# Kernel optimization log

Measured on AMD Instinct MI355X. Metric: run time of the kernel, lower is better.

Reference implementation:

```python
import jax, jax.numpy as jnp
import numpy as np

BS, C, H, W = 256, 512, 9, 9
D = 9           # spe_kerner (spectral attention kernel size)
SPA_HEAD = 64
HW = H * W      # 81; with spe_head=1, padsize=9 => share_head = 81 = HW
EPS = 1e-5


def _bn(x, p, axis=1):
    # inference-mode BatchNorm; p is (4, C) = [gamma, beta, running_mean, running_var]
    g, b, m, v = p
    sh = [1] * x.ndim; sh[axis] = -1
    return (x - m.reshape(sh)) * (g.reshape(sh) * jax.lax.rsqrt(v.reshape(sh) + EPS)) + b.reshape(sh)


def _conv2d(x, w, groups=1):
    return jax.lax.conv_general_dilated(
        x, w, (1, 1), 'SAME',
        dimension_numbers=('NCHW', 'OIHW', 'NCHW'),
        feature_group_count=groups)


def setup_inputs() -> dict:
    key = jax.random.key(0)
    ks = list(jax.random.split(key, 16))

    def rn(k, shape, s=0.05):
        return (jax.random.normal(k, shape) * s).astype(jnp.float32)

    def bnp(k, c):
        k1, k2, k3, k4 = jax.random.split(k, 4)
        g = jax.random.uniform(k1, (c,), minval=0.5, maxval=1.5)
        v = jax.random.uniform(k4, (c,), minval=0.5, maxval=1.5)
        return jnp.stack([g, rn(k2, (c,)), rn(k3, (c,)), v]).astype(jnp.float32)

    return {
        'x': jax.random.normal(ks[0], (BS, C, H, W), jnp.float32),
        'alpha': jnp.full((1,), 0.5, jnp.float32),
        # SaMCA params
        'sa_key_w': rn(ks[1], (C, 1, 3, 3)),                    # depthwise 3x3 key conv
        'sa_key_bn': bnp(ks[2], C),
        'sa_att_w1': rn(ks[3], (C, 2 * C // SPA_HEAD, 1, 1)),   # Conv2d(2C, C, 1, groups=64)
        'sa_att_bn': bnp(ks[4], C),
        'sa_att_w2': rn(ks[5], (SPA_HEAD, C // SPA_HEAD, 1, 1)),  # Conv2d(C, 64, 1, groups=64)
        'sa_att_b2': rn(ks[6], (SPA_HEAD,)),
        # SeMCA params
        'se_key_w': rn(ks[7], (HW, 1, D)),                      # depthwise Conv1d over spectral axis
        'se_key_b': rn(ks[8], (HW,)),
        'se_att_w1': rn(ks[9], (HW, 2 * HW)),                   # 1x1 Conv2d(162, 81), bias=False
        'se_att_bn': bnp(ks[10], HW),
        'se_att_w2': rn(ks[11], (D, HW)),                       # 1x1 Conv2d(81, 9)
        'se_att_b2': rn(ks[12], (D,)),
        'se_val_w': rn(ks[13], (C, 1, 3, 3)),                   # depthwise 3x3 value conv
        'se_val_b': rn(ks[14], (C,)),
    }


def reference(x, alpha, sa_key_w, sa_key_bn, sa_att_w1, sa_att_bn, sa_att_w2,
              sa_att_b2, se_key_w, se_key_b, se_att_w1, se_att_bn, se_att_w2,
              se_att_b2, se_val_w, se_val_b):
    bs, c, h, w = x.shape
    hw = h * w
    # ================= SeMCA (spectral attention) =================
    # convd_key: depthwise Conv1d over the spectral (channel) axis per pixel
    k = x.reshape(bs, c, hw).transpose(0, 2, 1)                 # (bs, hw, c)
    k1 = jax.lax.conv_general_dilated(
        k, se_key_w, (1,), [(D // 2, D // 2)],
        dimension_numbers=('NCH', 'OIH', 'NCH'),
        feature_group_count=hw) + se_key_b[None, :, None]
    k1 = k1.transpose(0, 2, 1).reshape(bs, c, h, w)
    # With padsize==img_size, Unfold(kernel=9) is a single full window -> flatten.
    q_flat = x.reshape(bs, 1, c * hw)
    k_flat = k1.reshape(bs, 1, c * hw)
    # torch layout-faithful: stack on dim 2 then reshape (bs, 2*hw, c)
    kq = jnp.stack([q_flat, k_flat], axis=2).reshape(bs, 2 * hw, c)
    a = jax.nn.relu(_bn(jnp.einsum('oi,bic->boc', se_att_w1, kq), se_att_bn))
    a = jnp.einsum('oi,bic->boc', se_att_w2, a) + se_att_b2[None, :, None]  # (bs, D, c)
    # repeat over all 81 positions + trivial block reshape (sidelen=1) -> same
    # D-vector at every pixel; softmax over the spectral kernel axis.
    a = jax.nn.softmax(a, axis=1)
    v = _conv2d(x, se_val_w, groups=c) + se_val_b[None, :, None, None]
    pad_v = jnp.pad(v, ((0, 0), (D // 2, D // 2), (0, 0), (0, 0)))
    # spectral sliding windows: v_win[b, i, k] = v_padded[b, i + k - D//2]
    v_win = jnp.stack([pad_v[:, k0:k0 + c] for k0 in range(D)], axis=2)  # (bs,c,D,h,w)
    out1 = jnp.einsum('bcdhw,bdc->bchw', v_win, a) + k1
    # ================= SaMCA (spatial attention) =================
    k1s = jax.nn.relu(_bn(_conv2d(x, sa_key_w, groups=c), sa_key_bn))
    # NOTE: value_embed in the original is computed then overwritten by x (dead code).
    kq2 = jnp.stack([k1s, x], axis=2).reshape(bs, 2 * c, h, w)  # interleaved channels
    a2 = jax.nn.relu(_bn(_conv2d(kq2, sa_att_w1, groups=SPA_HEAD), sa_att_bn))
    a2 = _conv2d(a2, sa_att_w2, groups=SPA_HEAD) + sa_att_b2[None, :, None, None]
    a2 = jax.nn.softmax(a2.reshape(bs, SPA_HEAD, hw), axis=-1)  # global spatial softmax
    k2 = jnp.broadcast_to(a2[:, :, None, :], (bs, SPA_HEAD, c // SPA_HEAD, hw)).reshape(bs, c, hw)
    out2 = k1s + (k2 * x.reshape(bs, c, hw)).reshape(bs, c, h, w)
    return alpha * out1 + (1.0 - alpha) * out2
```

## Files before the change

### kernel.cpp

```cpp
#include <hip/hip_runtime.h>
#include <hip/hip_fp16.h>

#define BSZ 256
#define CCH 512
#define HW_ 81
#define DD 9
#define CH 41472

#define WS_W1T   0
#define WS_TSE   13122
#define WS_S2    13203
#define WS_T2    13715
#define WS_W1S   14227
#define WS_T1    22419
#define WS_A2    22932
#define WS_ATT   1350036
#define WS_W1F   2529684
#define WS_TOTALP 22931
#define PREP_N   41363

typedef _Float16 half8 __attribute__((ext_vector_type(8)));
typedef float f32x4 __attribute__((ext_vector_type(4)));

__device__ __forceinline__ float h2f(unsigned short u) {
    return __half2float(__ushort_as_half(u));
}
__device__ __forceinline__ unsigned short f2h(float f) {
    return __half_as_ushort(__float2half(f));
}

__global__ void prep_kernel(const float* __restrict__ se_att_w1,
                            const float* __restrict__ se_att_bn,
                            const float* __restrict__ sa_key_bn,
                            const float* __restrict__ sa_att_w1,
                            const float* __restrict__ sa_att_bn,
                            float* __restrict__ ws) {
    int idx = blockIdx.x * blockDim.x + threadIdx.x;
    if (idx < 13122) {
        int r = idx / 81, o = idx % 81;
        float g = se_att_bn[o], v = se_att_bn[243 + o];
        float s = g * rsqrtf(v + 1e-5f);
        ws[WS_W1T + idx] = se_att_w1[o * 162 + r] * s;
    } else if (idx < 13203) {
        int o = idx - 13122;
        float g = se_att_bn[o], b = se_att_bn[81 + o], m = se_att_bn[162 + o], v = se_att_bn[243 + o];
        float s = g * rsqrtf(v + 1e-5f);
        ws[WS_TSE + o] = b - m * s;
    } else if (idx < 13715) {
        int c = idx - 13203;
        float g = sa_key_bn[c], v = sa_key_bn[1536 + c];
        ws[WS_S2 + c] = g * rsqrtf(v + 1e-5f);
    } else if (idx < 14227) {
        int c = idx - 13715;
        float g = sa_key_bn[c], b = sa_key_bn[512 + c], m = sa_key_bn[1024 + c], v = sa_key_bn[1536 + c];
        float s = g * rsqrtf(v + 1e-5f);
        ws[WS_T2 + c] = b - m * s;
    } else if (idx < 22419) {
        int e = idx - 14227;
        int o = e >> 4;
        float g = sa_att_bn[o], v = sa_att_bn[1536 + o];
        float s = g * rsqrtf(v + 1e-5f);
        ws[WS_W1S + e] = sa_att_w1[e] * s;
    } else if (idx < WS_TOTALP) {
        int o = idx - 22419;
        float g = sa_att_bn[o], b = sa_att_bn[512 + o], m = sa_att_bn[1024 + o], v = sa_att_bn[1536 + o];
        float s = g * rsqrtf(v + 1e-5f);
        ws[WS_T1 + o] = b - m * s;
    } else if (idx < PREP_N) {
        int e2 = (idx - WS_TOTALP) * 2;
        unsigned int packed = 0;
        #pragma unroll
        for (int q = 0; q < 2; ++q) {
            int e = e2 + q;
            int row = e / 192, k = e - row * 192;
            unsigned short val = 0;
            if (row < 81 && k < 162) {
                float g = se_att_bn[row], v = se_att_bn[243 + row];
                float s = g * rsqrtf(v + 1e-5f);
                val = f2h(se_att_w1[row * 162 + k] * s);
            }
            packed |= ((unsigned int)val) << (16 * q);
        }
        ((unsigned int*)(ws + WS_W1F))[idx - WS_TOTALP] = packed;
    }
}

__global__ __launch_bounds__(512, 4) void sa_kernel(
    const float* __restrict__ x,
    const float* __restrict__ sa_key_w,
    const float* __restrict__ sa_att_w2,
    const float* __restrict__ sa_att_b2,
    float* __restrict__ ws)
{
    __shared__ __align__(16) unsigned short xbh[128 * HW_];
    __shared__ float kvf[128 * HW_];
    __shared__ unsigned short wkbL[128 * DD];
    __shared__ float s2L[128];
    __shared__ float t2L[128];
    __shared__ float w1sL[128 * 16];
    __shared__ float saw2L[128];
    __shared__ float b2L[16];
    __shared__ float t1L[128];

    const int bid = blockIdx.x;
    const int b = bid >> 2;
    const int qr = bid & 3;
    const int c0 = qr * 128;
    const int t = threadIdx.x;

    {
        const float4* x4 = (const float4*)(x + (size_t)b * CH + (size_t)c0 * 81);
        for (int v = t; v < 128 * 81 / 4; v += 512) {
            float4 q = x4[v];
            ushort4 s4;
            s4.x = f2h(q.x); s4.y = f2h(q.y); s4.z = f2h(q.z); s4.w = f2h(q.w);
            *(ushort4*)(&xbh[4 * v]) = s4;
        }
        for (int v = t; v < 128 * DD; v += 512) wkbL[v] = f2h(sa_key_w[c0 * 9 + v]);
        if (t < 128) {
            s2L[t] = ws[WS_S2 + c0 + t];
            t2L[t] = ws[WS_T2 + c0 + t];
            saw2L[t] = sa_att_w2[c0 + t];
            t1L[t] = ws[WS_T1 + c0 + t];
        }
        for (int v = t; v < 128 * 16; v += 512) w1sL[v] = ws[WS_W1S + c0 * 16 + v];
        if (t < 16) b2L[t] = sa_att_b2[qr * 16 + t];
    }
    __syncthreads();

    #pragma unroll 2
    for (int idx = t; idx < 128 * 81; idx += 512) {
        int c = idx / 81, p = idx - 81 * c;
        int y = p / 9, xx = p - 9 * y;
        float conv = 0.f;
        #pragma unroll
        for (int ky = 0; ky < 3; ++ky) {
            int yy = y + ky - 1;
            if (yy < 0 || yy > 8) continue;
            #pragma unroll
            for (int kx = 0; kx < 3; ++kx) {
                int xc = xx + kx - 1;
                if (xc < 0 || xc > 8) continue;
                conv = fmaf(h2f(xbh[c * 81 + yy * 9 + xc]),
                            h2f(wkbL[c * 9 + ky * 3 + kx]), conv);
            }
        }
        kvf[idx] = fmaxf(conv * s2L[c] + t2L[c], 0.f);
    }
    __syncthreads();

    {
        const int g = t >> 5, sub = t & 31;
        const int cb = g * 8;
        float z[8][3];
        #pragma unroll
        for (int o = 0; o < 8; ++o)
            #pragma unroll
            for (int k = 0; k < 3; ++k)
                z[o][k] = t1L[cb + o];

        #pragma unroll 1
        for (int j = 0; j < 8; ++j) {
            float wk[8], wx[8];
            #pragma unroll
            for (int o = 0; o < 8; ++o) {
                wk[o] = w1sL[(cb + o) * 16 + 2 * j];
                wx[o] = w1sL[(cb + o) * 16 + 2 * j + 1];
            }
            const int rowb = (cb + j) * 81;
            #pragma unroll
            for (int k = 0; k < 3; ++k) {
                int p = sub + 32 * k;
                if (p > 80) p = 80;
                float kv = kvf[rowb + p];
                float xv = h2f(xbh[rowb + p]);
                #pragma unroll
                for (int o = 0; o < 8; ++o) {
                    z[o][k] = fmaf(wk[o], kv, z[o][k]);
                    z[o][k] = fmaf(wx[o], xv, z[o][k]);
                }
            }
        }

        float a2v[3];
        const float b2g = b2L[g];
        #pragma unroll
        for (int k = 0; k < 3; ++k) {
            float s = b2g;
            #pragma unroll
            for (int o = 0; o < 8; ++o)
                s = fmaf(saw2L[cb + o], fmaxf(z[o][k], 0.f), s);
            int p = sub + 32 * k;
            a2v[k] = (p < 81) ? s : -1e30f;
        }

        float m = a2v[0];
        #pragma unroll
        for (int k = 1; k < 3; ++k) m = fmaxf(m, a2v[k]);
        #pragma unroll
        for (int off = 1; off < 32; off <<= 1) m = fmaxf(m, __shfl_xor(m, off, 64));
        float ls = 0.f;
        float ev[3];
        #pragma unroll
        for (int k = 0; k < 3; ++k) { ev[k] = __expf(a2v[k] - m); ls += ev[k]; }
        #pragma unroll
        for (int off = 1; off < 32; off <<= 1) ls += __shfl_xor(ls, off, 64);
        float inv = 1.f / ls;

        float* a2out = ws + WS_A2 + (size_t)b * 5184 + (size_t)(qr * 16 + g) * 81;
        #pragma unroll
        for (int k = 0; k < 3; ++k) {
            int p = sub + 32 * k;
            if (p < 81) a2out[p] = ev[k] * inv;
        }
    }
}

__global__ __launch_bounds__(512) void se_kernel(
    const float* __restrict__ x,
    const float* __restrict__ se_key_w,
    const float* __restrict__ se_key_b,
    const float* __restrict__ se_att_w2,
    const float* __restrict__ se_att_b2,
    float* __restrict__ ws)
{
    __shared__ __align__(16) unsigned short xbh[CH];
    __shared__ __align__(16) unsigned short kqs[128 * 200];
    __shared__ float wseL[DD * HW_];
    __shared__ float bseL[HW_];
    __shared__ float w2L[DD * 96];
    __shared__ float tseL[96];

    const int b = blockIdx.x;
    const int t = threadIdx.x;
    const float* xb = x + (size_t)b * CH;

    for (int v = t; v < DD * HW_; v += 512) {
        int tau = v / 81, p = v - 81 * tau;
        wseL[tau * 81 + p] = se_key_w[p * 9 + tau];
    }
    if (t < HW_) bseL[t] = se_key_b[t];
    for (int v = t; v < DD * 96; v += 512) {
        int d = v / 96, row = v - 96 * d;
        w2L[v] = (row < 81) ? se_att_w2[d * 81 + row] : 0.f;
    }
    if (t < 96) tseL[t] = (t < 81) ? ws[WS_TSE + t] : 0.f;
    for (int v = t; v < 128 * 38; v += 512) {
        int k = v >> 7, jl = v & 127;
        kqs[jl * 200 + 162 + k] = 0;
    }
    {
        const float4* x4 = (const float4*)xb;
        #pragma unroll 4
        for (int v = t; v < CH / 4; v += 512) {
            float4 q = x4[v];
            ushort4 s4;
            s4.x = f2h(q.x); s4.y = f2h(q.y); s4.z = f2h(q.z); s4.w = f2h(q.w);
            *(ushort4*)(&xbh[4 * v]) = s4;
        }
    }
    __syncthreads();

    const int wv = t >> 6;
    const int lane = t & 63;
    const int quad = lane >> 4;
    const int l15 = lane & 15;
    const unsigned short* w1f = (const unsigned short*)(ws + WS_W1F);
    float* attout = ws + WS_ATT + (size_t)b * 4608;

    #pragma unroll 1
    for (int q = 0; q < 4; ++q) {
        const int c0 = q * 128;
        if (q) __syncthreads();

        {
            int k = t >> 7;
            const int jl = t & 127;
            #pragma unroll 2
            for (; k < 81; k += 4)
                kqs[jl * 200 + k] = xbh[k * 512 + c0 + jl];
        }
        {
            int kk = t >> 7;
            const int jl = t & 127;
            int e = kk * 512 + c0 + jl;
            int p = e % 81;
            #pragma unroll 2
            for (; kk < 81; kk += 4) {
                float s = bseL[p];
                if (e >= 324 && e < CH - 324) {
                    #pragma unroll
                    for (int tau = 0; tau < 9; ++tau)
                        s = fmaf(h2f(xbh[e - 324 + 81 * tau]), wseL[tau * 81 + p], s);
                } else {
                    #pragma unroll
                    for (int tau = 0; tau < 9; ++tau) {
                        int flat = e + (tau - 4) * 81;
                        if (flat >= 0 && flat < CH)
                            s = fmaf(h2f(xbh[flat]), wseL[tau * 81 + p], s);
                    }
                }
                kqs[jl * 200 + 81 + kk] = f2h(s);
                e += 2048;
                p += 23; if (p >= 81) p -= 81;
            }
        }
        __syncthreads();

        f32x4 acc[6];
        #pragma unroll
        for (int m = 0; m < 6; ++m) acc[m] = (f32x4){0.f, 0.f, 0.f, 0.f};

        #pragma unroll 1
        for (int pass = 0; pass < 6; ++pass) {
            half8 bfr = *(const half8*)&kqs[(wv * 16 + l15) * 200 + pass * 32 + quad * 8];
            #pragma unroll
            for (int m = 0; m < 6; ++m) {
                half8 afr = *(const half8*)&w1f[(m * 16 + l15) * 192 + pass * 32 + quad * 8];
                acc[m] = __builtin_amdgcn_mfma_f32_16x16x32_f16(afr, bfr, acc[m], 0, 0, 0);
            }
        }

        float pd[9];
        #pragma unroll
        for (int d = 0; d < 9; ++d) pd[d] = 0.f;
        #pragma unroll
        for (int m = 0; m < 6; ++m) {
            #pragma unroll
            for (int reg = 0; reg < 4; ++reg) {
                int row = m * 16 + quad * 4 + reg;
                float z = fmaxf(acc[m][reg] + tseL[row], 0.f);
                #pragma unroll
                for (int d = 0; d < 9; ++d)
                    pd[d] = fmaf(w2L[d * 96 + row], z, pd[d]);
            }
        }
        #pragma unroll
        for (int d = 0; d < 9; ++d) {
            pd[d] += __shfl_xor(pd[d], 16, 64);
            pd[d] += __shfl_xor(pd[d], 32, 64);
        }
        if (quad == 0) {
            int j = c0 + wv * 16 + l15;
            float ad[9];
            #pragma unroll
            for (int d = 0; d < 9; ++d) ad[d] = pd[d] + se_att_b2[d];
            float mm = ad[0];
            #pragma unroll
            for (int d = 1; d < 9; ++d) mm = fmaxf(mm, ad[d]);
            float ls = 0.f;
            #pragma unroll
            for (int d = 0; d < 9; ++d) { ad[d] = __expf(ad[d] - mm); ls += ad[d]; }
            float inv = 1.f / ls;
            #pragma unroll
            for (int d = 0; d < 9; ++d) attout[d * 512 + j] = ad[d] * inv;
        }
    }
}

__global__ __launch_bounds__(256, 4) void combine_kernel(
    const float* __restrict__ x,
    const float* __restrict__ alpha,
    const float* __restrict__ sa_key_w,
    const float* __restrict__ se_key_w,
    const float* __restrict__ se_key_b,
    const float* __restrict__ se_val_w,
    const float* __restrict__ se_val_b,
    const float* __restrict__ ws,
    float* __restrict__ out)
{
    __shared__ __align__(16) unsigned short xsh[72 * 81];
    __shared__ __align__(16) unsigned short vsh[72 * 81];
    __shared__ float wvL[72 * 9];
    __shared__ float bvL[72];
    __shared__ float wkL[64 * 9];
    __shared__ float s2L[64];
    __shared__ float t2L[64];
    __shared__ float wseT[9 * 81];
    __shared__ float bseL[81];
    __shared__ float attL[9 * 64];
    __shared__ float a2L[8 * 81];

    const int bid = blockIdx.x;
    const int b = bid >> 3;
    const int tile = bid & 7;
    const int c0 = tile * 64;
    const int t = threadIdx.x;
    const int f04 = ((c0 - 4) * 81) >> 2;

    {
        const float4* x4 = (const float4*)(x + (size_t)b * CH);
        for (int v = t; v < 1458; v += 256) {
            int g4 = f04 + v;
            float4 q = (g4 >= 0 && g4 < CH / 4) ? x4[g4]
                                                : (float4){0.f, 0.f, 0.f, 0.f};
            ushort4 s4;
            s4.x = f2h(q.x); s4.y = f2h(q.y); s4.z = f2h(q.z); s4.w = f2h(q.w);
            *(ushort4*)(&xsh[4 * v]) = s4;
        }
    }
    for (int idx = t; idx < 648; idx += 256) {
        int cc = c0 - 4 + idx / 9;
        wvL[idx] = (cc >= 0 && cc < 512) ? se_val_w[cc * 9 + idx % 9] : 0.f;
    }
    if (t < 72) {
        int cc = c0 - 4 + t;
        bvL[t] = (cc >= 0 && cc < 512) ? se_val_b[cc] : 0.f;
    }
    for (int idx = t; idx < 576; idx += 256) wkL[idx] = sa_key_w[c0 * 9 + idx];
    if (t < 64) { s2L[t] = ws[WS_S2 + c0 + t]; t2L[t] = ws[WS_T2 + c0 + t]; }
    for (int idx = t; idx < 729; idx += 256) {
        int p = idx / 9, tau = idx - 9 * p;
        wseT[tau * 81 + p] = se_key_w[idx];
    }
    if (t < 81) bseL[t] = se_key_b[t];
    for (int idx = t; idx < 576; idx += 256)
        attL[idx] = ws[WS_ATT + (size_t)b * 4608 + (idx >> 6) * 512 + c0 + (idx & 63)];
    for (int idx = t; idx < 648; idx += 256)
        a2L[idx] = ws[WS_A2 + (size_t)b * 5184 + tile * 648 + idx];
    __syncthreads();

    for (int idx = t; idx < 5832; idx += 256) {
        int i = idx / 81, p = idx - 81 * i;
        int cc = c0 - 4 + i;
        float r = 0.f;
        if (cc >= 0 && cc < 512) {
            int y = p / 9, xx = p - 9 * (p / 9);
            float s = 0.f;
            #pragma unroll
            for (int ky = 0; ky < 3; ++ky) {
                int yy = y + ky - 1;
                if (yy < 0 || yy > 8) continue;
                #pragma unroll
                for (int kx = 0; kx < 3; ++kx) {
                    int xc = xx + kx - 1;
                    if (xc < 0 || xc > 8) continue;
                    s = fmaf(h2f(xsh[i * 81 + yy * 9 + xc]), wvL[i * 9 + ky * 3 + kx], s);
                }
            }
            r = s + bvL[i];
        }
        vsh[idx] = f2h(r);
    }
    __syncthreads();

    const float av = alpha[0];
    const int cl = t >> 2, s = t & 3;
    float wk[9], attv[9];
    #pragma unroll
    for (int j = 0; j < 9; ++j) wk[j] = wkL[cl * 9 + j];
    #pragma unroll
    for (int d = 0; d < 9; ++d) attv[d] = attL[d * 64 + cl];
    const float s2 = s2L[cl], t2 = t2L[cl];
    const float* a2row = &a2L[(cl >> 3) * 81];
    float* outrow = out + (size_t)b * CH + (size_t)(c0 + cl) * 81;
    const int rowc = (cl + 4) * 81;

    #pragma unroll 1
    for (int k = 0; k < 21; ++k) {
        int p = s + 4 * k;
        if (p < 81) {
            int y = p / 9, xx = p - 9 * y;
            float sk = 0.f;
            #pragma unroll
            for (int ky = 0; ky < 3; ++ky) {
                int yy = y + ky - 1;
                if (yy < 0 || yy > 8) continue;
                #pragma unroll
                for (int kx = 0; kx < 3; ++kx) {
                    int xc = xx + kx - 1;
                    if (xc < 0 || xc > 8) continue;
                    sk = fmaf(h2f(xsh[rowc + yy * 9 + xc]), wk[ky * 3 + kx], sk);
                }
            }
            float k1s = fmaxf(sk * s2 + t2, 0.f);
            float o1 = 0.f;
            #pragma unroll
            for (int d = 0; d < 9; ++d)
                o1 = fmaf(h2f(vsh[(cl + d) * 81 + p]), attv[d], o1);
            float k1se = bseL[p];
            #pragma unroll
            for (int tau = 0; tau < 9; ++tau)
                k1se = fmaf(h2f(xsh[(cl + tau) * 81 + p]), wseT[tau * 81 + p], k1se);
            float out2 = k1s + a2row[p] * h2f(xsh[rowc + p]);
            outrow[p] = av * (o1 + k1se) + (1.f - av) * out2;
        }
    }
}

extern "C" void kernel_launch(void* const* d_in, const int* in_sizes, int n_in,
                              void* d_out, int out_size, void* d_ws, size_t ws_size,
                              hipStream_t stream) {
    const float* x          = (const float*)d_in[0];
    const float* alpha      = (const float*)d_in[1];
    const float* sa_key_w   = (const float*)d_in[2];
    const float* sa_key_bn  = (const float*)d_in[3];
    const float* sa_att_w1  = (const float*)d_in[4];
    const float* sa_att_bn  = (const float*)d_in[5];
    const float* sa_att_w2  = (const float*)d_in[6];
    const float* sa_att_b2  = (const float*)d_in[7];
    const float* se_key_w   = (const float*)d_in[8];
    const float* se_key_b   = (const float*)d_in[9];
    const float* se_att_w1  = (const float*)d_in[10];
    const float* se_att_bn  = (const float*)d_in[11];
    const float* se_att_w2  = (const float*)d_in[12];
    const float* se_att_b2  = (const float*)d_in[13];
    const float* se_val_w   = (const float*)d_in[14];
    const float* se_val_b   = (const float*)d_in[15];
    float* ws = (float*)d_ws;
    float* outp = (float*)d_out;

    prep_kernel<<<(PREP_N + 255) / 256, 256, 0, stream>>>(
        se_att_w1, se_att_bn, sa_key_bn, sa_att_w1, sa_att_bn, ws);
    sa_kernel<<<BSZ * 4, 512, 0, stream>>>(
        x, sa_key_w, sa_att_w2, sa_att_b2, ws);
    se_kernel<<<BSZ, 512, 0, stream>>>(
        x, se_key_w, se_key_b, se_att_w2, se_att_b2, ws);
    combine_kernel<<<BSZ * 8, 256, 0, stream>>>(
        x, alpha, sa_key_w, se_key_w, se_key_b, se_val_w, se_val_b, ws, outp);
}
```

Baseline: 314.7 us.

## Pad shared tiles to 12-wide rows and compute combine kernel per spatial row

Shared-memory x and value tiles, the spectral key weights, bias and spatial attention now use a padded layout with 12-element rows and 108-element channel stride. Each thread processes one whole 9-pixel row of one channel using vectorized row loads, which lets it reuse neighbouring rows across the 3x3 convolutions and the spectral sums. The goal is fewer scalar LDS reads and less index arithmetic per output. In exchange the kernel uses more LDS and registers, the global-to-shared scatter becomes scalar, the 4-blocks-per-CU occupancy hint is dropped, and output stores become short row writes with fewer active threads (576 row tasks).

```diff
diff --git a/kernel.cpp b/kernel.cpp
--- a/kernel.cpp
+++ b/kernel.cpp
@@ -358,7 +358,30 @@
     }
 }
 
-__global__ __launch_bounds__(256, 4) void combine_kernel(
+#define CS 108
+#define RS 12
+
+__device__ __forceinline__ void ldrow_h(const unsigned short* base, float* r) {
+    ushort4 a = *(const ushort4*)(base);
+    ushort4 bq = *(const ushort4*)(base + 4);
+    unsigned short c = base[8];
+    r[0] = h2f(a.x); r[1] = h2f(a.y); r[2] = h2f(a.z); r[3] = h2f(a.w);
+    r[4] = h2f(bq.x); r[5] = h2f(bq.y); r[6] = h2f(bq.z); r[7] = h2f(bq.w);
+    r[8] = h2f(c);
+}
+__device__ __forceinline__ void ldrow_f(const float* base, float* r) {
+    float4 a = *(const float4*)(base);
+    float4 bq = *(const float4*)(base + 4);
+    r[0] = a.x; r[1] = a.y; r[2] = a.z; r[3] = a.w;
+    r[4] = bq.x; r[5] = bq.y; r[6] = bq.z; r[7] = bq.w;
+    r[8] = base[8];
+}
+__device__ __forceinline__ void zrow(float* r) {
+    #pragma unroll
+    for (int xx = 0; xx < 9; ++xx) r[xx] = 0.f;
+}
+
+__global__ __launch_bounds__(256) void combine_kernel(
     const float* __restrict__ x,
     const float* __restrict__ alpha,
     const float* __restrict__ sa_key_w,
@@ -369,34 +392,39 @@
     const float* __restrict__ ws,
     float* __restrict__ out)
 {
-    __shared__ __align__(16) unsigned short xsh[72 * 81];
-    __shared__ __align__(16) unsigned short vsh[72 * 81];
+    __shared__ __align__(16) unsigned short xsh[72 * CS];
+    __shared__ __align__(16) unsigned short vsh[72 * CS];
+    __shared__ __align__(16) float wsePad[9 * CS];
+    __shared__ __align__(16) float bsePad[CS];
+    __shared__ __align__(16) float a2Pad[8 * CS];
     __shared__ float wvL[72 * 9];
     __shared__ float bvL[72];
     __shared__ float wkL[64 * 9];
     __shared__ float s2L[64];
     __shared__ float t2L[64];
-    __shared__ float wseT[9 * 81];
-    __shared__ float bseL[81];
     __shared__ float attL[9 * 64];
-    __shared__ float a2L[8 * 81];
 
     const int bid = blockIdx.x;
     const int b = bid >> 3;
     const int tile = bid & 7;
     const int c0 = tile * 64;
     const int t = threadIdx.x;
-    const int f04 = ((c0 - 4) * 81) >> 2;
+    const int f0 = (c0 - 4) * 81;
 
     {
-        const float4* x4 = (const float4*)(x + (size_t)b * CH);
-        for (int v = t; v < 1458; v += 256) {
-            int g4 = f04 + v;
-            float4 q = (g4 >= 0 && g4 < CH / 4) ? x4[g4]
-                                                : (float4){0.f, 0.f, 0.f, 0.f};
-            ushort4 s4;
-            s4.x = f2h(q.x); s4.y = f2h(q.y); s4.z = f2h(q.z); s4.w = f2h(q.w);
-            *(ushort4*)(&xsh[4 * v]) = s4;
+        const float* xg = x + (size_t)b * CH;
+        for (int v4 = t; v4 < 1458; v4 += 256) {
+            int lf = v4 * 4;
+            int gf = f0 + lf;
+            float4 q = (gf >= 0 && gf < CH) ? *(const float4*)(xg + gf)
+                                            : (float4){0.f, 0.f, 0.f, 0.f};
+            #pragma unroll
+            for (int j = 0; j < 4; ++j) {
+                int lfj = lf + j;
+                int i = lfj / 81, p = lfj - 81 * i;
+                int yy = p / 9, xx = p - 9 * yy;
+                xsh[i * CS + yy * RS + xx] = f2h(((const float*)&q)[j]);
+            }
         }
     }
     for (int idx = t; idx < 648; idx += 256) {
@@ -409,81 +437,119 @@
     }
     for (int idx = t; idx < 576; idx += 256) wkL[idx] = sa_key_w[c0 * 9 + idx];
     if (t < 64) { s2L[t] = ws[WS_S2 + c0 + t]; t2L[t] = ws[WS_T2 + c0 + t]; }
-    for (int idx = t; idx < 729; idx += 256) {
-        int p = idx / 9, tau = idx - 9 * p;
-        wseT[tau * 81 + p] = se_key_w[idx];
-    }
-    if (t < 81) bseL[t] = se_key_b[t];
+    for (int idx = t; idx < 972; idx += 256) {
+        int tau = idx / CS, r = idx - CS * tau;
+        int yy = r / RS, xx = r - RS * yy;
+        if (xx < 9) wsePad[idx] = se_key_w[(yy * 9 + xx) * 9 + tau];
+    }
+    if (t < CS) {
+        int yy = t / RS, xx = t - RS * yy;
+        if (xx < 9) bsePad[t] = se_key_b[yy * 9 + xx];
+    }
+    for (int idx = t; idx < 864; idx += 256) {
+        int g = idx / CS, r = idx - CS * g;
+        int yy = r / RS, xx = r - RS * yy;
+        if (xx < 9)
+            a2Pad[idx] = ws[WS_A2 + (size_t)b * 5184 + (size_t)(tile * 8 + g) * 81 + yy * 9 + xx];
+    }
     for (int idx = t; idx < 576; idx += 256)
         attL[idx] = ws[WS_ATT + (size_t)b * 4608 + (idx >> 6) * 512 + c0 + (idx & 63)];
-    for (int idx = t; idx < 648; idx += 256)
-        a2L[idx] = ws[WS_A2 + (size_t)b * 5184 + tile * 648 + idx];
     __syncthreads();
 
-    for (int idx = t; idx < 5832; idx += 256) {
-        int i = idx / 81, p = idx - 81 * i;
-        int cc = c0 - 4 + i;
-        float r = 0.f;
-        if (cc >= 0 && cc < 512) {
-            int y = p / 9, xx = p - 9 * (p / 9);
-            float s = 0.f;
-            #pragma unroll
-            for (int ky = 0; ky < 3; ++ky) {
-                int yy = y + ky - 1;
-                if (yy < 0 || yy > 8) continue;
+    #pragma unroll 1
+    for (int u = t; u < 648; u += 256) {
+        int i = u / 9, yy = u - 9 * i;
+        const int cb = i * CS;
+        float q0[9], q1[9], q2[9];
+        if (yy > 0) ldrow_h(&xsh[cb + (yy - 1) * RS], q0);
+        else zrow(q0);
+        ldrow_h(&xsh[cb + yy * RS], q1);
+        if (yy < 8) ldrow_h(&xsh[cb + (yy + 1) * RS], q2);
+        else zrow(q2);
+        float wv[9];
+        #pragma unroll
+        for (int j = 0; j < 9; ++j) wv[j] = wvL[i * 9 + j];
+        const float bv = bvL[i];
+        float o[9];
+        #pragma unroll
+        for (int xx = 0; xx < 9; ++xx) {
+            float s = bv;
+            #pragma unroll
+            for (int kx = 0; kx < 3; ++kx) {
+                int xc = xx + kx - 1;
+                if (xc >= 0 && xc <= 8) {
+                    s = fmaf(q0[xc], wv[kx], s);
+                    s = fmaf(q1[xc], wv[3 + kx], s);
+                    s = fmaf(q2[xc], wv[6 + kx], s);
+                }
+            }
+            o[xx] = s;
+        }
+        const int vb = cb + yy * RS;
+        ushort4 wA, wB;
+        wA.x = f2h(o[0]); wA.y = f2h(o[1]); wA.z = f2h(o[2]); wA.w = f2h(o[3]);
+        wB.x = f2h(o[4]); wB.y = f2h(o[5]); wB.z = f2h(o[6]); wB.w = f2h(o[7]);
+        *(ushort4*)(&vsh[vb]) = wA;
+        *(ushort4*)(&vsh[vb + 4]) = wB;
+        vsh[vb + 8] = f2h(o[8]);
+    }
+    __syncthreads();
+
+    const float av = alpha[0];
+    #pragma unroll 1
+    for (int u = t; u < 576; u += 256) {
+        int cl = u / 9, yy = u - 9 * cl;
+        const int rb = yy * RS;
+        float acc[9];
+        ldrow_f(&bsePad[rb], acc);
+        float r1[9];
+        #pragma unroll
+        for (int tau = 0; tau < 9; ++tau) {
+            float xr[9], wr[9];
+            ldrow_h(&xsh[(cl + tau) * CS + rb], xr);
+            ldrow_f(&wsePad[tau * CS + rb], wr);
+            #pragma unroll
+            for (int xx = 0; xx < 9; ++xx) acc[xx] = fmaf(xr[xx], wr[xx], acc[xx]);
+            if (tau == 4) {
                 #pragma unroll
-                for (int kx = 0; kx < 3; ++kx) {
-                    int xc = xx + kx - 1;
-                    if (xc < 0 || xc > 8) continue;
-                    s = fmaf(h2f(xsh[i * 81 + yy * 9 + xc]), wvL[i * 9 + ky * 3 + kx], s);
+                for (int xx = 0; xx < 9; ++xx) r1[xx] = xr[xx];
+            }
+        }
+        #pragma unroll
+        for (int d = 0; d < 9; ++d) {
+            float vr[9];
+            ldrow_h(&vsh[(cl + d) * CS + rb], vr);
+            const float ad = attL[d * 64 + cl];
+            #pragma unroll
+            for (int xx = 0; xx < 9; ++xx) acc[xx] = fmaf(vr[xx], ad, acc[xx]);
+        }
+        float r0[9], r2[9];
+        if (yy > 0) ldrow_h(&xsh[(cl + 4) * CS + rb - RS], r0);
+        else zrow(r0);
+        if (yy < 8) ldrow_h(&xsh[(cl + 4) * CS + rb + RS], r2);
+        else zrow(r2);
+        float wkr[9];
+        #pragma unroll
+        for (int j = 0; j < 9; ++j) wkr[j] = wkL[cl * 9 + j];
+        const float s2 = s2L[cl], t2v = t2L[cl];
+        float a2r[9];
+        ldrow_f(&a2Pad[(cl >> 3) * CS + rb], a2r);
+        float* orow = out + (size_t)b * CH + (size_t)(c0 + cl) * 81 + yy * 9;
+        #pragma unroll
+        for (int xx = 0; xx < 9; ++xx) {
+            float sk = 0.f;
+            #pragma unroll
+            for (int kx = 0; kx < 3; ++kx) {
+                int xc = xx + kx - 1;
+                if (xc >= 0 && xc <= 8) {
+                    sk = fmaf(r0[xc], wkr[kx], sk);
+                    sk = fmaf(r1[xc], wkr[3 + kx], sk);
+                    sk = fmaf(r2[xc], wkr[6 + kx], sk);
                 }
             }
-            r = s + bvL[i];
-        }
-        vsh[idx] = f2h(r);
-    }
-    __syncthreads();
-
-    const float av = alpha[0];
-    const int cl = t >> 2, s = t & 3;
-    float wk[9], attv[9];
-    #pragma unroll
-    for (int j = 0; j < 9; ++j) wk[j] = wkL[cl * 9 + j];
-    #pragma unroll
-    for (int d = 0; d < 9; ++d) attv[d] = attL[d * 64 + cl];
-    const float s2 = s2L[cl], t2 = t2L[cl];
-    const float* a2row = &a2L[(cl >> 3) * 81];
-    float* outrow = out + (size_t)b * CH + (size_t)(c0 + cl) * 81;
-    const int rowc = (cl + 4) * 81;
-
-    #pragma unroll 1
-    for (int k = 0; k < 21; ++k) {
-        int p = s + 4 * k;
-        if (p < 81) {
-            int y = p / 9, xx = p - 9 * y;
-            float sk = 0.f;
-            #pragma unroll
-            for (int ky = 0; ky < 3; ++ky) {
-                int yy = y + ky - 1;
-                if (yy < 0 || yy > 8) continue;
-                #pragma unroll
-                for (int kx = 0; kx < 3; ++kx) {
-                    int xc = xx + kx - 1;
-                    if (xc < 0 || xc > 8) continue;
-                    sk = fmaf(h2f(xsh[rowc + yy * 9 + xc]), wk[ky * 3 + kx], sk);
-                }
-            }
-            float k1s = fmaxf(sk * s2 + t2, 0.f);
-            float o1 = 0.f;
-            #pragma unroll
-            for (int d = 0; d < 9; ++d)
-                o1 = fmaf(h2f(vsh[(cl + d) * 81 + p]), attv[d], o1);
-            float k1se = bseL[p];
-            #pragma unroll
-            for (int tau = 0; tau < 9; ++tau)
-                k1se = fmaf(h2f(xsh[(cl + tau) * 81 + p]), wseT[tau * 81 + p], k1se);
-            float out2 = k1s + a2row[p] * h2f(xsh[rowc + p]);
-            outrow[p] = av * (o1 + k1se) + (1.f - av) * out2;
+            float k1s = fmaxf(sk * s2 + t2v, 0.f);
+            float out2 = k1s + a2r[xx] * r1[xx];
+            orow[xx] = av * acc[xx] + (1.f - av) * out2;
         }
     }
 }
```

After: 291.8 us. 7.3% less time.
